# Kernel optimization log

Measured on AMD Instinct MI355X. Metric: run time of the kernel, lower is better.

The kernel has to match this reference:

```python
import jax, jax.numpy as jnp
import numpy as np

B, N, IN_DIM, OUT_DIM, H = 8, 1024, 256, 256, 4
HD = OUT_DIM // H  # head_dim = 64
NEG = -1e9
EPS = 1e-5


def setup_inputs() -> dict:
    key = jax.random.key(0)
    ks = jax.random.split(key, 9)
    h = jax.random.normal(ks[0], (B, N, IN_DIM), dtype=jnp.float32)
    adj = jax.random.randint(ks[1], (N, N), 0, 2, dtype=jnp.int32)
    adj = adj.at[jnp.arange(N), jnp.arange(N)].set(1)  # self loops so no empty rows
    s = 1.0 / np.sqrt(IN_DIM)
    W = jax.random.uniform(ks[2], (H, IN_DIM, HD), jnp.float32, -s, s)
    sa = 1.0 / np.sqrt(2 * HD)
    a1 = jax.random.uniform(ks[3], (H, HD), jnp.float32, -sa, sa)
    a2 = jax.random.uniform(ks[4], (H, HD), jnp.float32, -sa, sa)
    sp = 1.0 / np.sqrt(OUT_DIM)
    proj_w = jax.random.uniform(ks[5], (OUT_DIM, OUT_DIM), jnp.float32, -sp, sp)
    proj_b = jax.random.uniform(ks[6], (OUT_DIM,), jnp.float32, -sp, sp)
    gamma = jnp.ones((OUT_DIM,), jnp.float32)
    beta = jnp.zeros((OUT_DIM,), jnp.float32)
    return {"h": h, "adj": adj, "W": W, "a1": a1, "a2": a2,
            "proj_w": proj_w, "proj_b": proj_b, "gamma": gamma, "beta": beta}


def reference(h, adj, W, a1, a2, proj_w, proj_b, gamma, beta):
    # Wh: [B,H,N,HD]
    Wh = jnp.einsum('bni,hid->bhnd', h, W)
    # Decompose a([Wh_i || Wh_j]) = a1.Wh_i + a2.Wh_j (same math as concat+linear)
    si = jnp.einsum('bhnd,hd->bhn', Wh, a1)  # [B,H,N]
    sj = jnp.einsum('bhnd,hd->bhn', Wh, a2)
    e = jax.nn.leaky_relu(si[:, :, :, None] + sj[:, :, None, :], 0.2)  # [B,H,N,N]
    mask = (adj == 0)  # [N,N]
    e = jnp.where(mask[None, None], NEG, e)
    alpha = jax.nn.softmax(e, axis=-1)
    out = jnp.einsum('bhnm,bhmd->bhnd', alpha, Wh)  # [B,H,N,HD]
    h_multi = out.transpose(0, 2, 1, 3).reshape(B, N, OUT_DIM)  # concat heads
    h_out = jnp.einsum('bnd,od->bno', h_multi, proj_w) + proj_b
    h_out = h_out + h  # residual (in_dim == out_dim)
    mu = jnp.mean(h_out, axis=-1, keepdims=True)
    var = jnp.mean(jnp.square(h_out - mu), axis=-1, keepdims=True)
    return (h_out - mu) * jax.lax.rsqrt(var + EPS) * gamma + beta
```

## Files before the change

### kernel.cpp

```cpp
#include <hip/hip_runtime.h>
#include <hip/hip_bf16.h>

#define NN 1024
#define LOG2E 1.44269504088896f

typedef __attribute__((ext_vector_type(8))) short short8;
typedef __attribute__((ext_vector_type(4))) float floatx4;
typedef __attribute__((ext_vector_type(4))) int intx4;
typedef __attribute__((ext_vector_type(2))) int intx2;

static __device__ __forceinline__ unsigned pk2(float f0, float f1) {
    unsigned u0 = __float_as_uint(f0) + 0x8000u;
    unsigned u1 = __float_as_uint(f1) + 0x8000u;
    return __builtin_amdgcn_perm(u1, u0, 0x07060302u);
}
static __device__ __forceinline__ short8 pk8(floatx4 v0, floatx4 v1) {
    union { intx4 i; short8 s; } u;
    u.i[0] = (int)pk2(v0[0], v0[1]); u.i[1] = (int)pk2(v0[2], v0[3]);
    u.i[2] = (int)pk2(v1[0], v1[1]); u.i[3] = (int)pk2(v1[2], v1[3]);
    return u.s;
}
static __device__ __forceinline__ void load_lds16(const void* gsrc, void* lds) {
    __builtin_amdgcn_global_load_lds(
        (const __attribute__((address_space(1))) void*)gsrc,
        (__attribute__((address_space(3))) void*)lds, 16, 0, 0);
}

__global__ __launch_bounds__(256) void prep_kernel(
    const float* __restrict__ W, const float* __restrict__ proj_w,
    const int* __restrict__ adj,
    __hip_bfloat16* __restrict__ WTb,
    __hip_bfloat16* __restrict__ pwb,
    unsigned* __restrict__ adjm)
{
    int blk = blockIdx.x, t = threadIdx.x;
    if (blk < 16) {
        int o = blk * 16 + (t >> 4);
        int hh = o >> 6, d = o & 63;
        #pragma unroll
        for (int kk = 0; kk < 16; ++kk) {
            int k = (t & 15) + 16 * kk;
            WTb[(size_t)o * 256 + k] = __float2bfloat16(W[((size_t)hh * 256 + k) * 64 + d]);
        }
    } else if (blk < 32) {
        size_t base = (size_t)(blk - 16) * 4096 + (size_t)t * 16;
        #pragma unroll
        for (int k = 0; k < 16; k += 8) {
            floatx4 v0 = *(const floatx4*)(proj_w + base + k);
            floatx4 v1 = *(const floatx4*)(proj_w + base + k + 4);
            *(short8*)(pwb + base + k) = pk8(v0, v1);
        }
    } else {
        int n = (blk - 32) * 8 + (t >> 5);
        int wd = t & 31;
        const int* arow = adj + (size_t)n * NN + wd * 32;
        unsigned bits = 0;
        #pragma unroll
        for (int j4 = 0; j4 < 8; ++j4) {
            intx4 v = *(const intx4*)(arow + j4 * 4);
            #pragma unroll
            for (int j = 0; j < 4; ++j) if (v[j] != 0) bits |= (1u << (j4 * 4 + j));
        }
        adjm[(size_t)n * 32 + wd] = bits;
    }
}

__global__ __launch_bounds__(256) void wh_kernel(
    const float* __restrict__ h,
    const __hip_bfloat16* __restrict__ WTb,
    const float* __restrict__ a1, const float* __restrict__ a2,
    __hip_bfloat16* __restrict__ WhT,
    float* __restrict__ si, float* __restrict__ sj)
{
    int t = threadIdx.x;
    int w = t >> 6, l = t & 63;
    int rl = l & 15, q = l >> 4;
    int r0 = blockIdx.x * 16;
    int bb = r0 >> 10, n0 = r0 & 1023;

    __shared__ __align__(16) __hip_bfloat16 bst[4][2][4096];
    __shared__ float redsi[4][4][16];
    __shared__ float redsj[4][4][16];

    short8 af[8];
    const float* Arow = h + (size_t)(r0 + rl) * 256 + q * 8;
    #pragma unroll
    for (int k0 = 0; k0 < 8; ++k0) {
        floatx4 v0 = *(const floatx4*)(Arow + k0 * 32);
        floatx4 v1 = *(const floatx4*)(Arow + k0 * 32 + 4);
        af[k0] = pk8(v0, v1);
    }

    #pragma unroll
    for (int k = 0; k < 8; ++k) {
        int row = k * 2 + (l >> 5);
        int g = (l & 31) ^ (row & 7);
        load_lds16(WTb + (size_t)w * 4096 + row * 256 + g * 8, &bst[w][0][k * 512]);
    }

    #pragma unroll
    for (int j = 0; j < 4; ++j) {
        int cur = j & 1;
        if (j < 3) {
            int ctn = w + 4 * (j + 1);
            #pragma unroll
            for (int k = 0; k < 8; ++k) {
                int row = k * 2 + (l >> 5);
                int g = (l & 31) ^ (row & 7);
                load_lds16(WTb + (size_t)ctn * 4096 + row * 256 + g * 8, &bst[w][cur ^ 1][k * 512]);
            }
        }
        floatx4 acc = {0.f, 0.f, 0.f, 0.f};
        #pragma unroll
        for (int k0 = 0; k0 < 8; ++k0) {
            int p = ((k0 << 2) + q) ^ (rl & 7);
            short8 bf = *(const short8*)(&bst[w][cur][rl * 256 + p * 8]);
            acc = __builtin_amdgcn_mfma_f32_16x16x32_bf16(af[k0], bf, acc, 0, 0, 0);
        }

        intx2 pr;
        pr[0] = (int)pk2(acc[0], acc[1]);
        pr[1] = (int)pk2(acc[2], acc[3]);
        *(intx2*)(WhT + ((size_t)(bb * 4 + j) * 64 + w * 16 + rl) * NN + n0 + q * 4) = pr;

        float av1 = a1[j * 64 + w * 16 + rl] * LOG2E;
        float av2 = a2[j * 64 + w * 16 + rl] * LOG2E;
        #pragma unroll
        for (int i = 0; i < 4; ++i) {
            float p1 = acc[i] * av1, p2 = acc[i] * av2;
            #pragma unroll
            for (int off = 1; off < 16; off <<= 1) {
                p1 += __shfl_xor(p1, off, 64);
                p2 += __shfl_xor(p2, off, 64);
            }
            if (rl == 0) { redsi[w][j][q * 4 + i] = p1; redsj[w][j][q * 4 + i] = p2; }
        }
    }
    __syncthreads();

    if (t < 64) {
        int head = t >> 4, row = t & 15;
        si[(size_t)(bb * 4 + head) * NN + n0 + row] =
            redsi[0][head][row] + redsi[1][head][row] + redsi[2][head][row] + redsi[3][head][row];
    } else if (t < 128) {
        int u = t - 64;
        int head = u >> 4, row = u & 15;
        sj[(size_t)(bb * 4 + head) * NN + n0 + row] =
            redsj[0][head][row] + redsj[1][head][row] + redsj[2][head][row] + redsj[3][head][row];
    }
}

__global__ __launch_bounds__(256) void attn_proj_kernel(
    const unsigned* __restrict__ adjm,
    const __hip_bfloat16* __restrict__ WhT,
    const float* __restrict__ si, const float* __restrict__ sj,
    const __hip_bfloat16* __restrict__ pwb,
    const float* __restrict__ h,
    const float* __restrict__ proj_b, const float* __restrict__ gamma,
    const float* __restrict__ beta,
    float* __restrict__ out)
{
    __shared__ __align__(16) char smem[75264];
    auto bst   = reinterpret_cast<__hip_bfloat16 (*)[2][8192 / 2]>(smem);
    auto pl    = reinterpret_cast<__hip_bfloat16 (*)[16][72]>(smem + 65536);
    auto rinvs = reinterpret_cast<float (*)[16]>(smem + 74752);
    auto pbst  = reinterpret_cast<__hip_bfloat16 (*)[16][264]>(smem);
    auto hm    = reinterpret_cast<__hip_bfloat16 (*)[264]>(smem + 65536);
    auto red   = reinterpret_cast<float (*)[4][16]>(smem + 74752);

    int bx = blockIdx.x, t = threadIdx.x;
    int w = t >> 6, l = t & 63;
    int rl = l & 15, q = l >> 4;
    int b = bx >> 6, n0 = (bx & 63) * 16;
    int bh = b * 4 + w;
    int r0 = bx * 16;

    int r = l >> 2, cg = l & 3;
    float sii = si[(size_t)bh * NN + n0 + r];
    const float* sjr = sj + (size_t)bh * NN;
    const unsigned* amrow = adjm + (size_t)(n0 + r) * 32;

    float lsum = 0.f;
    floatx4 acc[4] = { {0,0,0,0}, {0,0,0,0}, {0,0,0,0}, {0,0,0,0} };

    const __hip_bfloat16* Bhead = WhT + (size_t)bh * 64 * NN;
    int lrow = l >> 3;
    int lgrp = (l & 7) ^ lrow;

    #pragma unroll
    for (int k = 0; k < 8; ++k)
        load_lds16(Bhead + (size_t)(k * 8 + lrow) * NN + lgrp * 8, &bst[w][0][k * 512]);

    #pragma unroll
    for (int it = 0; it < 16; ++it) {
        int m0 = it * 64;
        int cur = it & 1;
        if (it < 15) {
            int m1 = m0 + 64;
            #pragma unroll
            for (int k = 0; k < 8; ++k)
                load_lds16(Bhead + (size_t)(k * 8 + lrow) * NN + m1 + lgrp * 8,
                           &bst[w][cur ^ 1][k * 512]);
        }
        {
            int mb = m0 + cg * 16;
            unsigned bits = amrow[(m0 >> 5) + (cg >> 1)] >> ((cg & 1) * 16);
            #pragma unroll
            for (int c4 = 0; c4 < 4; ++c4) {
                floatx4 s4 = *(const floatx4*)(sjr + mb + c4 * 4);
                float pv[4];
                #pragma unroll
                for (int k = 0; k < 4; ++k) {
                    float x = sii + s4[k];
                    x = fmaxf(x, 0.2f * x);
                    x = ((bits >> (c4 * 4 + k)) & 1u) ? x : -1e9f;
                    pv[k] = exp2f(x);
                    lsum += pv[k];
                }
                intx2 two;
                two[0] = (int)pk2(pv[0], pv[1]);
                two[1] = (int)pk2(pv[2], pv[3]);
                *(intx2*)(&pl[w][r][cg * 16 + c4 * 4]) = two;
            }
        }
        #pragma unroll
        for (int ks = 0; ks < 2; ++ks) {
            short8 afr = *(const short8*)(&pl[w][rl][ks * 32 + q * 8]);
            #pragma unroll
            for (int dt = 0; dt < 4; ++dt) {
                int p = ((ks << 2) + q) ^ (rl & 7);
                short8 bfr = *(const short8*)(&bst[w][cur][(dt * 16 + rl) * 64 + p * 8]);
                acc[dt] = __builtin_amdgcn_mfma_f32_16x16x32_bf16(afr, bfr, acc[dt], 0, 0, 0);
            }
        }
    }

    lsum += __shfl_xor(lsum, 1, 64);
    lsum += __shfl_xor(lsum, 2, 64);
    if (cg == 0) rinvs[w][r] = 1.f / lsum;
    float riv[4];
    #pragma unroll
    for (int i = 0; i < 4; ++i) riv[i] = rinvs[w][q * 4 + i];

    short8 psreg[8], pnreg[8];
    {
        const __hip_bfloat16* src = pwb + (size_t)w * 16 * 256;
        #pragma unroll
        for (int k = 0; k < 8; ++k) psreg[k] = *(const short8*)(src + k * 512 + l * 8);
    }

    __syncthreads();
    #pragma unroll
    for (int dt = 0; dt < 4; ++dt) {
        #pragma unroll
        for (int i = 0; i < 4; ++i) {
            unsigned uv = (__float_as_uint(acc[dt][i] * riv[i]) + 0x8000u) >> 16;
            hm[q * 4 + i][w * 64 + dt * 16 + rl] = __ushort_as_bfloat16((unsigned short)uv);
        }
    }
    __syncthreads();

    short8 paf[8];
    #pragma unroll
    for (int k0 = 0; k0 < 8; ++k0) paf[k0] = *(const short8*)(&hm[rl][q * 8 + k0 * 32]);

    floatx4 pacc[4];
    #pragma unroll
    for (int j = 0; j < 4; ++j) {
        if (j < 3) {
            const __hip_bfloat16* src = pwb + (size_t)(w + 4 * (j + 1)) * 16 * 256;
            #pragma unroll
            for (int k = 0; k < 8; ++k) pnreg[k] = *(const short8*)(src + k * 512 + l * 8);
        }
        #pragma unroll
        for (int k = 0; k < 8; ++k)
            *(short8*)(&pbst[w][k * 2 + (l >> 5)][(l & 31) * 8]) = psreg[k];
        floatx4 a = {0.f, 0.f, 0.f, 0.f};
        #pragma unroll
        for (int k0 = 0; k0 < 8; ++k0) {
            short8 bf = *(const short8*)(&pbst[w][rl][q * 8 + k0 * 32]);
            a = __builtin_amdgcn_mfma_f32_16x16x32_bf16(paf[k0], bf, a, 0, 0, 0);
        }
        pacc[j] = a;
        #pragma unroll
        for (int z = 0; z < 8; ++z) psreg[z] = pnreg[z];
    }

    float ps[4] = {0.f, 0.f, 0.f, 0.f};
    #pragma unroll
    for (int j = 0; j < 4; ++j) {
        int col = (w + j * 4) * 16 + rl;
        float pb = proj_b[col];
        #pragma unroll
        for (int i = 0; i < 4; ++i) {
            float v = pacc[j][i] + pb + h[(size_t)(r0 + q * 4 + i) * 256 + col];
            pacc[j][i] = v;
            ps[i] += v;
        }
    }
    #pragma unroll
    for (int i = 0; i < 4; ++i) {
        float s = ps[i];
        #pragma unroll
        for (int off = 1; off < 16; off <<= 1) s += __shfl_xor(s, off, 64);
        ps[i] = s;
    }
    if (rl == 0) {
        for (int i = 0; i < 4; ++i) red[0][w][q * 4 + i] = ps[i];
    }
    __syncthreads();
    float mu[4];
    #pragma unroll
    for (int i = 0; i < 4; ++i) {
        int row = q * 4 + i;
        mu[i] = (red[0][0][row] + red[0][1][row] + red[0][2][row] + red[0][3][row]) * (1.f / 256.f);
    }
    float vs[4] = {0.f, 0.f, 0.f, 0.f};
    #pragma unroll
    for (int j = 0; j < 4; ++j) {
        #pragma unroll
        for (int i = 0; i < 4; ++i) { float cv = pacc[j][i] - mu[i]; vs[i] += cv * cv; }
    }
    #pragma unroll
    for (int i = 0; i < 4; ++i) {
        float s = vs[i];
        #pragma unroll
        for (int off = 1; off < 16; off <<= 1) s += __shfl_xor(s, off, 64);
        vs[i] = s;
    }
    if (rl == 0) {
        for (int i = 0; i < 4; ++i) red[1][w][q * 4 + i] = vs[i];
    }
    __syncthreads();
    float rs[4];
    #pragma unroll
    for (int i = 0; i < 4; ++i) {
        int row = q * 4 + i;
        float var = (red[1][0][row] + red[1][1][row] + red[1][2][row] + red[1][3][row]) * (1.f / 256.f);
        rs[i] = rsqrtf(var + 1e-5f);
    }
    #pragma unroll
    for (int j = 0; j < 4; ++j) {
        int col = (w + j * 4) * 16 + rl;
        float g = gamma[col], be = beta[col];
        #pragma unroll
        for (int i = 0; i < 4; ++i)
            out[(size_t)(r0 + q * 4 + i) * 256 + col] = (pacc[j][i] - mu[i]) * rs[i] * g + be;
    }
}

extern "C" void kernel_launch(void* const* d_in, const int* in_sizes, int n_in,
                              void* d_out, int out_size, void* d_ws, size_t ws_size,
                              hipStream_t stream) {
    const float* h      = (const float*)d_in[0];
    const int*   adj    = (const int*)d_in[1];
    const float* W      = (const float*)d_in[2];
    const float* a1     = (const float*)d_in[3];
    const float* a2     = (const float*)d_in[4];
    const float* proj_w = (const float*)d_in[5];
    const float* proj_b = (const float*)d_in[6];
    const float* gamma  = (const float*)d_in[7];
    const float* beta   = (const float*)d_in[8];
    float* out = (float*)d_out;

    char* ws = (char*)d_ws;
    __hip_bfloat16* WhT = (__hip_bfloat16*)ws;   ws += (size_t)32 * 64 * NN * 2;
    __hip_bfloat16* WTb = (__hip_bfloat16*)ws;   ws += 256 * 256 * 2;
    __hip_bfloat16* pwb = (__hip_bfloat16*)ws;   ws += 256 * 256 * 2;
    float* si = (float*)ws;                      ws += (size_t)32 * NN * 4;
    float* sj = (float*)ws;                      ws += (size_t)32 * NN * 4;
    unsigned* adjm = (unsigned*)ws;              ws += (size_t)NN * 32 * 4;

    prep_kernel<<<160, 256, 0, stream>>>(W, proj_w, adj, WTb, pwb, adjm);
    wh_kernel<<<512, 256, 0, stream>>>(h, WTb, a1, a2, WhT, si, sj);
    attn_proj_kernel<<<512, 256, 0, stream>>>(adjm, WhT, si, sj, pwb, h, proj_b, gamma, beta, out);
}
```

Measured before the change: 120.9 us.

## Single-buffer LDS staging with explicit waitcnts to cut shared memory and raise occupancy

Replaces the double-buffered LDS staging in the projection and attention kernels with a single buffer per wave. Explicit vmcnt/lgkmcnt waits order each load against the matching reads. This drops the attention kernel's LDS from about 75KB to about 43KB so more blocks can be resident per CU. The projection weight staging moves from register round-trips to direct global-to-LDS loads with a swizzle. The cost is that loads no longer overlap compute within a wave, since each tile is waited on before use, so latency must be hidden by the extra occupancy.

```diff
diff --git a/kernel.cpp b/kernel.cpp
--- a/kernel.cpp
+++ b/kernel.cpp
@@ -8,6 +8,9 @@
 typedef __attribute__((ext_vector_type(4))) float floatx4;
 typedef __attribute__((ext_vector_type(4))) int intx4;
 typedef __attribute__((ext_vector_type(2))) int intx2;
+
+#define WAIT_VM0()   asm volatile("s_waitcnt vmcnt(0)" ::: "memory")
+#define WAIT_LGKM0() asm volatile("s_waitcnt lgkmcnt(0)" ::: "memory")
 
 static __device__ __forceinline__ unsigned pk2(float f0, float f1) {
     unsigned u0 = __float_as_uint(f0) + 0x8000u;
@@ -78,7 +81,7 @@
     int r0 = blockIdx.x * 16;
     int bb = r0 >> 10, n0 = r0 & 1023;
 
-    __shared__ __align__(16) __hip_bfloat16 bst[4][2][4096];
+    __shared__ __align__(16) __hip_bfloat16 bst[4][4096];
     __shared__ float redsi[4][4][16];
     __shared__ float redsj[4][4][16];
 
@@ -95,27 +98,28 @@
     for (int k = 0; k < 8; ++k) {
         int row = k * 2 + (l >> 5);
         int g = (l & 31) ^ (row & 7);
-        load_lds16(WTb + (size_t)w * 4096 + row * 256 + g * 8, &bst[w][0][k * 512]);
-    }
-
-    #pragma unroll
-    for (int j = 0; j < 4; ++j) {
-        int cur = j & 1;
+        load_lds16(WTb + (size_t)w * 4096 + row * 256 + g * 8, &bst[w][k * 512]);
+    }
+
+    #pragma unroll
+    for (int j = 0; j < 4; ++j) {
+        WAIT_VM0();
+        floatx4 acc = {0.f, 0.f, 0.f, 0.f};
+        #pragma unroll
+        for (int k0 = 0; k0 < 8; ++k0) {
+            int p = ((k0 << 2) + q) ^ (rl & 7);
+            short8 bf = *(const short8*)(&bst[w][rl * 256 + p * 8]);
+            acc = __builtin_amdgcn_mfma_f32_16x16x32_bf16(af[k0], bf, acc, 0, 0, 0);
+        }
+        WAIT_LGKM0();
         if (j < 3) {
             int ctn = w + 4 * (j + 1);
             #pragma unroll
             for (int k = 0; k < 8; ++k) {
                 int row = k * 2 + (l >> 5);
                 int g = (l & 31) ^ (row & 7);
-                load_lds16(WTb + (size_t)ctn * 4096 + row * 256 + g * 8, &bst[w][cur ^ 1][k * 512]);
-            }
-        }
-        floatx4 acc = {0.f, 0.f, 0.f, 0.f};
-        #pragma unroll
-        for (int k0 = 0; k0 < 8; ++k0) {
-            int p = ((k0 << 2) + q) ^ (rl & 7);
-            short8 bf = *(const short8*)(&bst[w][cur][rl * 256 + p * 8]);
-            acc = __builtin_amdgcn_mfma_f32_16x16x32_bf16(af[k0], bf, acc, 0, 0, 0);
+                load_lds16(WTb + (size_t)ctn * 4096 + row * 256 + g * 8, &bst[w][k * 512]);
+            }
         }
 
         intx2 pr;
@@ -160,13 +164,13 @@
     const float* __restrict__ beta,
     float* __restrict__ out)
 {
-    __shared__ __align__(16) char smem[75264];
-    auto bst   = reinterpret_cast<__hip_bfloat16 (*)[2][8192 / 2]>(smem);
-    auto pl    = reinterpret_cast<__hip_bfloat16 (*)[16][72]>(smem + 65536);
-    auto rinvs = reinterpret_cast<float (*)[16]>(smem + 74752);
-    auto pbst  = reinterpret_cast<__hip_bfloat16 (*)[16][264]>(smem);
-    auto hm    = reinterpret_cast<__hip_bfloat16 (*)[264]>(smem + 65536);
-    auto red   = reinterpret_cast<float (*)[4][16]>(smem + 74752);
+    __shared__ __align__(16) char smem[42752];
+    auto bst   = reinterpret_cast<__hip_bfloat16 (*)[4096]>(smem);
+    auto pl    = reinterpret_cast<__hip_bfloat16 (*)[16][72]>(smem + 32768);
+    auto rinvs = reinterpret_cast<float (*)[16]>(smem + 41984);
+    auto pbst  = reinterpret_cast<__hip_bfloat16 (*)[4096]>(smem);
+    auto hm    = reinterpret_cast<__hip_bfloat16 (*)[264]>(smem + 32768);
+    auto red   = reinterpret_cast<float (*)[4][16]>(smem + 42240);
 
     int bx = blockIdx.x, t = threadIdx.x;
     int w = t >> 6, l = t & 63;
@@ -187,21 +191,11 @@
     int lrow = l >> 3;
     int lgrp = (l & 7) ^ lrow;
 
-    #pragma unroll
-    for (int k = 0; k < 8; ++k)
-        load_lds16(Bhead + (size_t)(k * 8 + lrow) * NN + lgrp * 8, &bst[w][0][k * 512]);
-
-    #pragma unroll
     for (int it = 0; it < 16; ++it) {
         int m0 = it * 64;
-        int cur = it & 1;
-        if (it < 15) {
-            int m1 = m0 + 64;
-            #pragma unroll
-            for (int k = 0; k < 8; ++k)
-                load_lds16(Bhead + (size_t)(k * 8 + lrow) * NN + m1 + lgrp * 8,
-                           &bst[w][cur ^ 1][k * 512]);
-        }
+        #pragma unroll
+        for (int k = 0; k < 8; ++k)
+            load_lds16(Bhead + (size_t)(k * 8 + lrow) * NN + m0 + lgrp * 8, &bst[w][k * 512]);
         {
             int mb = m0 + cg * 16;
             unsigned bits = amrow[(m0 >> 5) + (cg >> 1)] >> ((cg & 1) * 16);
@@ -223,16 +217,18 @@
                 *(intx2*)(&pl[w][r][cg * 16 + c4 * 4]) = two;
             }
         }
+        WAIT_VM0();
         #pragma unroll
         for (int ks = 0; ks < 2; ++ks) {
             short8 afr = *(const short8*)(&pl[w][rl][ks * 32 + q * 8]);
             #pragma unroll
             for (int dt = 0; dt < 4; ++dt) {
                 int p = ((ks << 2) + q) ^ (rl & 7);
-                short8 bfr = *(const short8*)(&bst[w][cur][(dt * 16 + rl) * 64 + p * 8]);
+                short8 bfr = *(const short8*)(&bst[w][(dt * 16 + rl) * 64 + p * 8]);
                 acc[dt] = __builtin_amdgcn_mfma_f32_16x16x32_bf16(afr, bfr, acc[dt], 0, 0, 0);
             }
         }
+        WAIT_LGKM0();
     }
 
     lsum += __shfl_xor(lsum, 1, 64);
@@ -242,11 +238,11 @@
     #pragma unroll
     for (int i = 0; i < 4; ++i) riv[i] = rinvs[w][q * 4 + i];
 
-    short8 psreg[8], pnreg[8];
-    {
-        const __hip_bfloat16* src = pwb + (size_t)w * 16 * 256;
-        #pragma unroll
-        for (int k = 0; k < 8; ++k) psreg[k] = *(const short8*)(src + k * 512 + l * 8);
+    #pragma unroll
+    for (int k = 0; k < 8; ++k) {
+        int row = k * 2 + (l >> 5);
+        int g = (l & 31) ^ (row & 7);
+        load_lds16(pwb + (size_t)w * 4096 + row * 256 + g * 8, &pbst[w][k * 512]);
     }
 
     __syncthreads();
@@ -267,23 +263,25 @@
     floatx4 pacc[4];
     #pragma unroll
     for (int j = 0; j < 4; ++j) {
+        WAIT_VM0();
+        floatx4 a = {0.f, 0.f, 0.f, 0.f};
+        #pragma unroll
+        for (int k0 = 0; k0 < 8; ++k0) {
+            int p = ((k0 << 2) + q) ^ (rl & 7);
+            short8 bf = *(const short8*)(&pbst[w][rl * 256 + p * 8]);
+            a = __builtin_amdgcn_mfma_f32_16x16x32_bf16(paf[k0], bf, a, 0, 0, 0);
+        }
+        pacc[j] = a;
+        WAIT_LGKM0();
         if (j < 3) {
-            const __hip_bfloat16* src = pwb + (size_t)(w + 4 * (j + 1)) * 16 * 256;
-            #pragma unroll
-            for (int k = 0; k < 8; ++k) pnreg[k] = *(const short8*)(src + k * 512 + l * 8);
-        }
-        #pragma unroll
-        for (int k = 0; k < 8; ++k)
-            *(short8*)(&pbst[w][k * 2 + (l >> 5)][(l & 31) * 8]) = psreg[k];
-        floatx4 a = {0.f, 0.f, 0.f, 0.f};
-        #pragma unroll
-        for (int k0 = 0; k0 < 8; ++k0) {
-            short8 bf = *(const short8*)(&pbst[w][rl][q * 8 + k0 * 32]);
-            a = __builtin_amdgcn_mfma_f32_16x16x32_bf16(paf[k0], bf, a, 0, 0, 0);
-        }
-        pacc[j] = a;
-        #pragma unroll
-        for (int z = 0; z < 8; ++z) psreg[z] = pnreg[z];
+            int ctn = w + 4 * (j + 1);
+            #pragma unroll
+            for (int k = 0; k < 8; ++k) {
+                int row = k * 2 + (l >> 5);
+                int g = (l & 31) ^ (row & 7);
+                load_lds16(pwb + (size_t)ctn * 4096 + row * 256 + g * 8, &pbst[w][k * 512]);
+            }
+        }
     }
 
     float ps[4] = {0.f, 0.f, 0.f, 0.f};
```

Measured after the change: 120.3 us. No clear change (-0.5%).
